# Kernel optimization log

Measured on AMD Instinct MI355X. Metric: run time of the kernel, lower is better.

Reference implementation:

```python
import jax, jax.numpy as jnp
import numpy as np

N_NODES = 100_000
N_EDGES = 1_600_000
N_SPECIES = 4
ATTR = 16
HID = 32
NBASIS = 8
SH = 4  # l=0 (1) + l=1 (3)
R_CUT = 5.0


def setup_inputs() -> dict:
    key = jax.random.key(0)
    ks = jax.random.split(key, 13)
    inp = {
        "x": jax.random.randint(ks[0], (N_NODES,), 0, N_SPECIES),
        "pos": jax.random.normal(ks[1], (N_NODES, 3), jnp.float32),
        "edge_index": jax.random.randint(ks[2], (2, N_EDGES), 0, N_NODES),
        "cell": jax.random.normal(ks[3], (3, 3), jnp.float32),
        "cell_offset": jax.random.randint(ks[4], (N_EDGES, 3), 0, 3),
        "elem_embed": jax.random.normal(ks[5], (N_SPECIES, ATTR), jnp.float32),
        "W_embed": jax.random.normal(ks[6], (ATTR, HID), jnp.float32) * 0.25,
        "Wr": jax.random.normal(ks[7], (3, NBASIS, HID * SH), jnp.float32) * 0.25,
        "br": jax.random.normal(ks[8], (3, HID * SH), jnp.float32) * 0.1,
        "Wout": jax.random.normal(ks[9], (3, HID, HID), jnp.float32) * 0.18,
        "Wsc": jax.random.normal(ks[10], (3, ATTR, HID), jnp.float32) * 0.25,
        "P1": jax.random.normal(ks[11], (HID, 32), jnp.float32) * 0.18,
        "P2": jax.random.normal(ks[12], (32, 4), jnp.float32) * 0.18,
    }
    return inp


def _radial_basis(r, r_safe):
    # Bessel basis with smooth polynomial cutoff (p = 6)
    n = jnp.arange(1, NBASIS + 1, dtype=r.dtype)  # [NBASIS]
    rb = jnp.sin(n * jnp.pi * r / R_CUT) / r_safe  # [E, NBASIS]
    u = r / R_CUT
    p = 6.0
    env = 1.0 - (p + 1) * (p + 2) / 2 * u ** p + p * (p + 2) * u ** (p + 1) - p * (p + 1) / 2 * u ** (p + 2)
    env = jnp.where(u < 1.0, env, 0.0)
    return rb * env


def reference(x, pos, edge_index, cell, cell_offset, elem_embed, W_embed, Wr, br, Wout, Wsc, P1, P2):
    src, dst = edge_index[0], edge_index[1]
    n_nodes = pos.shape[0]
    n_edges = src.shape[0]

    # PBC shift vectors (offsets in {-1,0,1})
    period_vec = (cell_offset.astype(pos.dtype) - 1.0) @ cell  # [E,3]

    # node attributes / initial embedding
    x_attr = elem_embed[x]          # [N, ATTR]
    h = x_attr @ W_embed            # [N, HID]

    # edge attributes: vectors, lengths, spherical harmonics (l<=1)
    edge_vec = pos[dst] - pos[src] + period_vec            # [E,3]
    r = jnp.linalg.norm(edge_vec, axis=-1, keepdims=True)  # [E,1]
    r_safe = jnp.maximum(r, 1e-9)
    unit = edge_vec / r_safe
    edge_sh = jnp.concatenate([jnp.ones_like(r), unit], axis=-1)  # [E,SH]

    rbf = _radial_basis(r, r_safe)  # [E, NBASIS]

    # 3 message-passing convolutions
    for l in range(3):
        w = (rbf @ Wr[l] + br[l]).reshape(n_edges, HID, SH)          # per-edge TP weights
        msg = jnp.einsum('eh,es,ehs->eh', h[src], edge_sh, w)        # gather + edge compute
        agg = jax.ops.segment_sum(msg, dst, num_segments=n_nodes)    # scatter-reduce
        h = jax.nn.silu(agg @ Wout[l] + x_attr @ Wsc[l])

    # post-conv readout
    h = jax.nn.silu(h @ P1) @ P2  # [N,4]
    energies = h[:, 0]
    forces = h[:, 1:4]
    return energies, forces
```

## Files before the change

kernel.cpp:

```cpp
#include <hip/hip_runtime.h>
#include <hip/hip_bf16.h>
#include <math.h>

#define NN 100000
#define NE 1600000
#define HIDD 32
#define ATTR_ 16
#define NB 8
#define NBUK 782
#define CAP 2560
#define WPB 10
#define SCHUNK 4096
#define PAD_PAY (13<<17)

typedef __hip_bfloat16 bf16;
typedef _Float16 half8  __attribute__((ext_vector_type(8)));
typedef _Float16 half2v __attribute__((ext_vector_type(2)));
typedef float    f32x4  __attribute__((ext_vector_type(4)));

__device__ __forceinline__ float silu_(float v){ return v / (1.f + expf(-v)); }

__global__ void k_init(const int* __restrict__ x, const float* __restrict__ elem,
                       const float* __restrict__ Wemb, bf16* __restrict__ h,
                       float* __restrict__ agg){
  int idx = blockIdx.x*256 + threadIdx.x;
  if (idx >= NN*HIDD) return;
  int node = idx >> 5, hh = idx & 31;
  int xi = x[node];
  float acc = 0.f;
  #pragma unroll
  for (int a=0; a<ATTR_; a++) acc += elem[xi*ATTR_+a] * Wemb[a*HIDD+hh];
  h[idx] = __float2bfloat16(acc);
  agg[idx] = 0.f;
}

__global__ void k_binit(int* __restrict__ bcur){
  int i = blockIdx.x*256 + threadIdx.x;
  if (i < NBUK) bcur[i] = i*CAP;
}

__global__ void __launch_bounds__(256) k_bscatter(
    const int* __restrict__ ei, const int* __restrict__ coff,
    int* __restrict__ bcur, int* __restrict__ pairs){
  __shared__ int lh[NBUK];
  __shared__ int gb[NBUK];
  __shared__ int sbr[SCHUNK];
  __shared__ int spay[SCHUNK];
  const int t = threadIdx.x;
  const int base = blockIdx.x * SCHUNK;
  for (int i=t; i<NBUK; i+=256) lh[i] = 0;
  __syncthreads();
  for (int rr=0; rr<SCHUNK; rr+=256){
    int e = base + rr + t;
    if (e < NE){
      int src = ei[e], dst = ei[NE + e];
      int code = coff[e*3+0] + 3*coff[e*3+1] + 9*coff[e*3+2];
      int b = dst >> 7;
      int rank = atomicAdd(&lh[b], 1);
      sbr[rr+t]  = (b<<16) | rank;
      spay[rr+t] = src | (code<<17) | ((dst & 127)<<22);
    }
  }
  __syncthreads();
  for (int i=t; i<NBUK; i+=256){
    int c = lh[i];
    gb[i] = c ? atomicAdd(&bcur[i], c) : 0;
  }
  __syncthreads();
  for (int rr=0; rr<SCHUNK; rr+=256){
    int e = base + rr + t;
    if (e < NE){
      int br = sbr[rr+t];
      int b = br >> 16;
      int p = gb[b] + (br & 0xFFFF);
      if (p < (b+1)*CAP) pairs[p] = spay[rr+t];
    }
  }
}

__global__ void __launch_bounds__(256) k_fsort(
    const int* __restrict__ pairs, const int* __restrict__ bcur,
    int* __restrict__ es){
  __shared__ int spay[CAP];
  __shared__ int hist[128];
  __shared__ int cur[128];
  const int b = blockIdx.x, t = threadIdx.x;
  const int base = b*CAP;
  int K = bcur[b] - base; if (K > CAP) K = CAP; if (K < 0) K = 0;
  if (t < 128) hist[t] = 0;
  __syncthreads();
  for (int i=t; i<K; i+=256){
    int pay = pairs[base + i];
    spay[i] = pay;
    atomicAdd(&hist[(pay>>22) & 127], 1);
  }
  __syncthreads();
  if (t < 128) cur[t] = hist[t];
  __syncthreads();
  #pragma unroll
  for (int off=1; off<128; off<<=1){
    int u = (t >= off && t < 128) ? cur[t-off] : 0;
    __syncthreads();
    if (t < 128) cur[t] += u;
    __syncthreads();
  }
  if (t < 128) cur[t] -= hist[t];
  __syncthreads();
  for (int i=t; i<K; i+=256){
    int pay = spay[i];
    int p = base + atomicAdd(&cur[(pay>>22) & 127], 1);
    es[p] = pay;
  }
  for (int i=K+t; i<CAP; i+=256) es[base+i] = PAD_PAY;
}

__global__ void __launch_bounds__(256) k_edge8(
    const int* __restrict__ es, const int* __restrict__ bcur,
    const float* __restrict__ pos, const float* __restrict__ cell,
    const float* __restrict__ Wr_l, const float* __restrict__ br_l,
    const bf16* __restrict__ h, float* __restrict__ agg){
  __shared__ _Float16 Gs[256][40];
  __shared__ float ssh[256][4];
  __shared__ int ssrc[256];
  __shared__ int sdst[256];
  __shared__ _Float16 W2T[32][32];
  __shared__ float scell[9];
  const int t = threadIdx.x;

  int blk;
  {
    const int nwg = gridDim.x;
    int q = nwg >> 3, r = nwg & 7;
    int xcd = blockIdx.x & 7, lidx = blockIdx.x >> 3;
    blk = (xcd < r) ? (xcd*(q+1) + lidx) : (r*(q+1) + (xcd-r)*q + lidx);
  }
  const int b = blk / WPB, w = blk - b*WPB;
  const int base0 = b*CAP;
  int K = bcur[b] - base0; if (K > CAP) K = CAP;
  const int rem = K - w*256;
  if (rem <= 0) return;
  const int remc = rem < 256 ? rem : 256;

  if (t < 9) scell[t] = cell[t];
  {
    int hh2 = t >> 3, kq = t & 7;
    float4 w4 = *reinterpret_cast<const float4*>(Wr_l + kq*128 + hh2*4);
    W2T[hh2][kq*4+0] = (_Float16)w4.x;
    W2T[hh2][kq*4+1] = (_Float16)w4.y;
    W2T[hh2][kq*4+2] = (_Float16)w4.z;
    W2T[hh2][kq*4+3] = (_Float16)w4.w;
  }

  const int j = base0 + w*256 + t;
  const int pay = es[j];
  const int srcn = pay & 0x1FFFF;
  const int dstn = (b<<7) + ((pay>>22) & 127);
  ssrc[t] = srcn; sdst[t] = dstn;
  float pdx = pos[dstn*3+0], pdy = pos[dstn*3+1], pdz = pos[dstn*3+2];
  float psx = pos[srcn*3+0], psy = pos[srcn*3+1], psz = pos[srcn*3+2];
  __syncthreads();

  const int g = t >> 5, hh = t & 31, base = g*32;
  const unsigned short* hu = reinterpret_cast<const unsigned short*>(h);
  unsigned short hb[32];
  #pragma unroll
  for (int k=0; k<32; k++)
    hb[k] = hu[(size_t)ssrc[base+k]*HIDD + hh];

  {
    int code = (pay >> 17) & 31;
    int q = code / 3;
    float c0 = (float)(code - 3*q - 1);
    float c1 = (float)(q - 3*(q/3) - 1);
    float c2 = (float)(q/3 - 1);
    float vx = pdx - psx + c0*scell[0]+c1*scell[3]+c2*scell[6];
    float vy = pdy - psy + c0*scell[1]+c1*scell[4]+c2*scell[7];
    float vz = pdz - psz + c0*scell[2]+c1*scell[5]+c2*scell[8];
    float r  = sqrtf(vx*vx + vy*vy + vz*vz);
    float rs = fmaxf(r, 1e-9f);
    float u  = r * 0.2f;
    float env = 0.f;
    if (u < 1.f){
      float u2=u*u, u3=u2*u, u6=u3*u3, u7=u6*u, u8=u7*u;
      env = 1.f - 28.f*u6 + 48.f*u7 - 21.f*u8;
    }
    float sc = env / rs;
    float s1, c1t;
    __sincosf(0.62831853071795864769f * r, &s1, &c1t);
    float twoc = 2.f*c1t;
    float inv = 1.f / rs;
    float ux = vx*inv, uy = vy*inv, uz = vz*inv;
    float sp = 0.f, sn = s1;
    #pragma unroll
    for (int bb=0; bb<NB; bb++){
      float rb = sn*sc;
      half2v p0 = { (_Float16)rb,      (_Float16)(rb*ux) };
      half2v p1 = { (_Float16)(rb*uy), (_Float16)(rb*uz) };
      *reinterpret_cast<half2v*>(&Gs[t][bb*4])   = p0;
      *reinterpret_cast<half2v*>(&Gs[t][bb*4+2]) = p1;
      float nx = twoc*sn - sp; sp = sn; sn = nx;
    }
    float4 sh4 = make_float4(1.f, ux, uy, uz);
    *reinterpret_cast<float4*>(ssh[t]) = sh4;
  }

  asm volatile("s_waitcnt lgkmcnt(0)" ::: "memory");
  __builtin_amdgcn_s_barrier();
  __builtin_amdgcn_sched_barrier(0);

  {
    const int wv = t >> 6, l = t & 63;
    const int lrow = l & 15, lk = l >> 4;
    half8 b0 = *reinterpret_cast<half8*>(&W2T[lrow][lk*8]);
    half8 b1 = *reinterpret_cast<half8*>(&W2T[16+lrow][lk*8]);
    float4 br0 = *reinterpret_cast<const float4*>(br_l + 4*lrow);
    float4 br1 = *reinterpret_cast<const float4*>(br_l + 4*(16+lrow));
    const f32x4 zz = {0.f,0.f,0.f,0.f};
    #pragma unroll
    for (int m=0; m<4; m++){
      half8 a = *reinterpret_cast<half8*>(&Gs[(wv*4+m)*16 + lrow][lk*8]);
      f32x4 c0 = __builtin_amdgcn_mfma_f32_16x16x32_f16(a, b0, zz, 0, 0, 0);
      f32x4 c1 = __builtin_amdgcn_mfma_f32_16x16x32_f16(a, b1, zz, 0, 0, 0);
      #pragma unroll
      for (int r=0; r<4; r++){
        int edge = (wv*4+m)*16 + lk*4 + r;
        float4 sh4 = *reinterpret_cast<float4*>(ssh[edge]);
        float bias0 = sh4.x*br0.x + sh4.y*br0.y + sh4.z*br0.z + sh4.w*br0.w;
        float bias1 = sh4.x*br1.x + sh4.y*br1.y + sh4.z*br1.z + sh4.w*br1.w;
        Gs[edge][lrow]    = (_Float16)(c0[r] + bias0);
        Gs[edge][16+lrow] = (_Float16)(c1[r] + bias1);
      }
    }
  }

  float accv = 0.f;
  int curd = sdst[base];
  #pragma unroll
  for (int k=0; k<32; k++){
    const int idx = base + k;
    int dst = sdst[idx];
    bool ok = idx < remc;
    if (ok && dst != curd){ atomicAdd(agg + (size_t)curd*HIDD + hh, accv); accv = 0.f; curd = dst; }
    float hv = __uint_as_float(((unsigned)hb[k]) << 16);
    float cvf = (float)Gs[idx][hh];
    if (ok) accv += hv * cvf;
  }
  if (accv != 0.f) atomicAdd(agg + (size_t)curd*HIDD + hh, accv);
}

__global__ void __launch_bounds__(256) k_edge(
    const float* __restrict__ pos, const int* __restrict__ ei,
    const float* __restrict__ cell, const int* __restrict__ coff,
    const float* __restrict__ Wr_l, const float* __restrict__ br_l,
    const bf16* __restrict__ h, float* __restrict__ agg){
  __shared__ float sfeat[8][12];
  __shared__ int   snode[8][2];
  const int e0 = blockIdx.x * 8;
  const int t  = threadIdx.x;
  if (t < 8){
    int e = e0 + t;
    int src = ei[e], dst = ei[NE + e];
    snode[t][0] = src; snode[t][1] = dst;
    float c0 = (float)(coff[e*3+0] - 1);
    float c1 = (float)(coff[e*3+1] - 1);
    float c2 = (float)(coff[e*3+2] - 1);
    float vx = pos[dst*3+0]-pos[src*3+0] + c0*cell[0]+c1*cell[3]+c2*cell[6];
    float vy = pos[dst*3+1]-pos[src*3+1] + c0*cell[1]+c1*cell[4]+c2*cell[7];
    float vz = pos[dst*3+2]-pos[src*3+2] + c0*cell[2]+c1*cell[5]+c2*cell[8];
    float r  = sqrtf(vx*vx+vy*vy+vz*vz);
    float rs = fmaxf(r, 1e-9f);
    float u  = r * 0.2f;
    float env = 0.f;
    if (u < 1.f){
      float u2=u*u, u3=u2*u, u6=u3*u3, u7=u6*u, u8=u7*u;
      env = 1.f - 28.f*u6 + 48.f*u7 - 21.f*u8;
    }
    float sc = env / rs;
    #pragma unroll
    for (int b=0; b<NB; b++)
      sfeat[t][b] = sinf((float)(b+1) * 3.14159265358979323846f * u) * sc;
    float inv = 1.f / rs;
    sfeat[t][8]  = 1.f;
    sfeat[t][9]  = vx*inv;
    sfeat[t][10] = vy*inv;
    sfeat[t][11] = vz*inv;
  }
  __syncthreads();
  const int el = t >> 5, hh = t & 31;
  const int src = snode[el][0], dst = snode[el][1];
  float hs = __bfloat162float(h[(size_t)src*HIDD + hh]);
  float4 acc = *reinterpret_cast<const float4*>(br_l + 4*hh);
  #pragma unroll
  for (int b=0; b<NB; b++){
    float rb = sfeat[el][b];
    float4 w = *reinterpret_cast<const float4*>(Wr_l + b*128 + 4*hh);
    acc.x += rb*w.x; acc.y += rb*w.y; acc.z += rb*w.z; acc.w += rb*w.w;
  }
  float c = acc.x*sfeat[el][8] + acc.y*sfeat[el][9]
          + acc.z*sfeat[el][10] + acc.w*sfeat[el][11];
  atomicAdd(agg + (size_t)dst*HIDD + hh, hs*c);
}

__global__ void k_node(const int* __restrict__ x, const float* __restrict__ elem,
                       const float* __restrict__ Wout_l, const float* __restrict__ Wsc_l,
                       bf16* __restrict__ h, float* __restrict__ agg){
  int idx = blockIdx.x*256 + threadIdx.x;
  if (idx >= NN*HIDD) return;
  int node = idx >> 5, hh = idx & 31;
  int xi = x[node];
  const float* arow = agg + (size_t)node*HIDD;
  float acc = 0.f;
  #pragma unroll
  for (int i=0; i<HIDD; i++) acc += arow[i] * Wout_l[i*HIDD+hh];
  #pragma unroll
  for (int a=0; a<ATTR_; a++) acc += elem[xi*ATTR_+a] * Wsc_l[a*HIDD+hh];
  h[idx] = __float2bfloat16(silu_(acc));
  agg[idx] = 0.f;
}

__global__ void __launch_bounds__(256) k_final2(
    const bf16* __restrict__ h, const float* __restrict__ P1,
    const float* __restrict__ P2, float* __restrict__ out){
  __shared__ float sP1[32][32];
  __shared__ float sh[8][32];
  const int t = threadIdx.x;
  {
    float4 v = reinterpret_cast<const float4*>(P1)[t];
    int r = (t*4) >> 5, c = (t*4) & 31;
    sP1[r][c]   = v.x; sP1[r][c+1] = v.y;
    sP1[r][c+2] = v.z; sP1[r][c+3] = v.w;
  }
  const int node0 = blockIdx.x * 8;
  ((float*)sh)[t] = __bfloat162float(h[(size_t)node0*HIDD + t]);
  __syncthreads();
  const int g = t >> 5, j = t & 31;
  const int node = node0 + g;
  float tj = 0.f;
  #pragma unroll
  for (int i=0; i<32; i++) tj += sh[g][i] * sP1[i][j];
  tj = silu_(tj);
  float4 p2 = reinterpret_cast<const float4*>(P2)[j];
  float o0 = tj*p2.x, o1 = tj*p2.y, o2 = tj*p2.z, o3 = tj*p2.w;
  #pragma unroll
  for (int m=1; m<32; m<<=1){
    o0 += __shfl_xor(o0, m);
    o1 += __shfl_xor(o1, m);
    o2 += __shfl_xor(o2, m);
    o3 += __shfl_xor(o3, m);
  }
  if (j == 0){
    out[node]            = o0;
    out[NN + node*3 + 0] = o1;
    out[NN + node*3 + 1] = o2;
    out[NN + node*3 + 2] = o3;
  }
}

extern "C" void kernel_launch(void* const* d_in, const int* in_sizes, int n_in,
                              void* d_out, int out_size, void* d_ws, size_t ws_size,
                              hipStream_t stream){
  const int*   x    = (const int*)  d_in[0];
  const float* pos  = (const float*)d_in[1];
  const int*   ei   = (const int*)  d_in[2];
  const float* cell = (const float*)d_in[3];
  const int*   coff = (const int*)  d_in[4];
  const float* elem = (const float*)d_in[5];
  const float* Wemb = (const float*)d_in[6];
  const float* Wr   = (const float*)d_in[7];
  const float* br   = (const float*)d_in[8];
  const float* Wout = (const float*)d_in[9];
  const float* Wsc  = (const float*)d_in[10];
  const float* P1   = (const float*)d_in[11];
  const float* P2   = (const float*)d_in[12];
  float* out = (float*)d_out;

  char* w = (char*)d_ws;
  bf16*  h    = (bf16*)w;  w += (size_t)NN*HIDD*2;
  float* agg  = (float*)w; w += (size_t)NN*HIDD*4;
  int*   bcur = (int*)w;   w += (size_t)1024*4;
  int*   es   = (int*)w;   w += (size_t)NBUK*CAP*4;
  const size_t need = (size_t)(w - (char*)d_ws);
  const bool fast = (ws_size >= need);
  int* pairs = (int*)agg;

  if (fast){
    k_binit<<<(NBUK+255)/256, 256, 0, stream>>>(bcur);
    k_bscatter<<<(NE + SCHUNK-1)/SCHUNK, 256, 0, stream>>>(ei, coff, bcur, pairs);
    k_fsort<<<NBUK, 256, 0, stream>>>(pairs, bcur, es);
  }
  k_init<<<(NN*HIDD+255)/256, 256, 0, stream>>>(x, elem, Wemb, h, agg);
  for (int l=0; l<3; l++){
    if (fast){
      k_edge8<<<NBUK*WPB, 256, 0, stream>>>(es, bcur, pos, cell,
                                            Wr + (size_t)l*NB*HIDD*4, br + (size_t)l*HIDD*4,
                                            h, agg);
    } else {
      k_edge<<<NE/8, 256, 0, stream>>>(pos, ei, cell, coff,
                                       Wr + (size_t)l*NB*HIDD*4, br + (size_t)l*HIDD*4,
                                       h, agg);
    }
    k_node<<<(NN*HIDD+255)/256, 256, 0, stream>>>(x, elem,
                                       Wout + (size_t)l*HIDD*HIDD, Wsc + (size_t)l*ATTR_*HIDD,
                                       h, agg);
  }
  k_final2<<<NN/8, 256, 0, stream>>>(h, P1, P2, out);
}
```

Baseline: 342.5 us.

## Compact sorted edges globally and replace LDS staging with wave shuffles

Adds a single-block prefix scan over bucket counts so the sorted edge list is stored densely, with an explicit per-edge destination array. This removes the padded per-bucket slots, so the edge kernel launches exactly NE/256 blocks with no early exit or validity masks. Source ids, destination ids and unit vectors are now passed between lanes with __shfl instead of shared-memory arrays, which drops several LDS buffers and one barrier. The cost is an extra tiny scan kernel and an extra 4-byte destination read per edge in each layer; it also relies on NE being a multiple of 256 and on no bucket overflowing CAP.

```diff
diff --git a/kernel.cpp b/kernel.cpp
--- a/kernel.cpp
+++ b/kernel.cpp
@@ -9,9 +9,7 @@
 #define NB 8
 #define NBUK 782
 #define CAP 2560
-#define WPB 10
 #define SCHUNK 4096
-#define PAD_PAY (13<<17)
 
 typedef __hip_bfloat16 bf16;
 typedef _Float16 half8  __attribute__((ext_vector_type(8)));
@@ -78,19 +76,38 @@
   }
 }
 
+__global__ void __launch_bounds__(1024) k_gscan(const int* __restrict__ bcur,
+                                               int* __restrict__ goff){
+  __shared__ int s[1024];
+  const int t = threadIdx.x;
+  int v = 0;
+  if (t < NBUK){ v = bcur[t] - t*CAP; if (v > CAP) v = CAP; if (v < 0) v = 0; }
+  s[t] = v; __syncthreads();
+  #pragma unroll
+  for (int off=1; off<1024; off<<=1){
+    int u = (t >= off) ? s[t-off] : 0;
+    __syncthreads();
+    s[t] += u;
+    __syncthreads();
+  }
+  if (t < NBUK) goff[t] = s[t] - v;
+}
+
 __global__ void __launch_bounds__(256) k_fsort(
     const int* __restrict__ pairs, const int* __restrict__ bcur,
-    int* __restrict__ es){
+    const int* __restrict__ goff,
+    int* __restrict__ es, int* __restrict__ dsts){
   __shared__ int spay[CAP];
   __shared__ int hist[128];
   __shared__ int cur[128];
   const int b = blockIdx.x, t = threadIdx.x;
-  const int base = b*CAP;
-  int K = bcur[b] - base; if (K > CAP) K = CAP; if (K < 0) K = 0;
+  const int sbase = b*CAP;
+  int K = bcur[b] - sbase; if (K > CAP) K = CAP; if (K < 0) K = 0;
+  const int gbase = goff[b];
   if (t < 128) hist[t] = 0;
   __syncthreads();
   for (int i=t; i<K; i+=256){
-    int pay = pairs[base + i];
+    int pay = pairs[sbase + i];
     spay[i] = pay;
     atomicAdd(&hist[(pay>>22) & 127], 1);
   }
@@ -106,25 +123,23 @@
   }
   if (t < 128) cur[t] -= hist[t];
   __syncthreads();
+  const int node0 = b << 7;
   for (int i=t; i<K; i+=256){
     int pay = spay[i];
-    int p = base + atomicAdd(&cur[(pay>>22) & 127], 1);
-    es[p] = pay;
-  }
-  for (int i=K+t; i<CAP; i+=256) es[base+i] = PAD_PAY;
-}
-
-__global__ void __launch_bounds__(256) k_edge8(
-    const int* __restrict__ es, const int* __restrict__ bcur,
+    int loc = (pay>>22) & 127;
+    int p = gbase + atomicAdd(&cur[loc], 1);
+    es[p]   = pay;
+    dsts[p] = node0 + loc;
+  }
+}
+
+__global__ void __launch_bounds__(256) k_edge9(
+    const int* __restrict__ es, const int* __restrict__ dsts,
     const float* __restrict__ pos, const float* __restrict__ cell,
     const float* __restrict__ Wr_l, const float* __restrict__ br_l,
     const bf16* __restrict__ h, float* __restrict__ agg){
   __shared__ _Float16 Gs[256][40];
-  __shared__ float ssh[256][4];
-  __shared__ int ssrc[256];
-  __shared__ int sdst[256];
   __shared__ _Float16 W2T[32][32];
-  __shared__ float scell[9];
   const int t = threadIdx.x;
 
   int blk;
@@ -134,14 +149,11 @@
     int xcd = blockIdx.x & 7, lidx = blockIdx.x >> 3;
     blk = (xcd < r) ? (xcd*(q+1) + lidx) : (r*(q+1) + (xcd-r)*q + lidx);
   }
-  const int b = blk / WPB, w = blk - b*WPB;
-  const int base0 = b*CAP;
-  int K = bcur[b] - base0; if (K > CAP) K = CAP;
-  const int rem = K - w*256;
-  if (rem <= 0) return;
-  const int remc = rem < 256 ? rem : 256;
-
-  if (t < 9) scell[t] = cell[t];
+
+  const int j = blk*256 + t;
+  const int pay = es[j];
+  const int dstn = dsts[j];
+  const int srcn = pay & 0x1FFFF;
   {
     int hh2 = t >> 3, kq = t & 7;
     float4 w4 = *reinterpret_cast<const float4*>(Wr_l + kq*128 + hh2*4);
@@ -150,32 +162,33 @@
     W2T[hh2][kq*4+2] = (_Float16)w4.z;
     W2T[hh2][kq*4+3] = (_Float16)w4.w;
   }
-
-  const int j = base0 + w*256 + t;
-  const int pay = es[j];
-  const int srcn = pay & 0x1FFFF;
-  const int dstn = (b<<7) + ((pay>>22) & 127);
-  ssrc[t] = srcn; sdst[t] = dstn;
   float pdx = pos[dstn*3+0], pdy = pos[dstn*3+1], pdz = pos[dstn*3+2];
   float psx = pos[srcn*3+0], psy = pos[srcn*3+1], psz = pos[srcn*3+2];
-  __syncthreads();
-
-  const int g = t >> 5, hh = t & 31, base = g*32;
+
+  asm volatile("s_waitcnt lgkmcnt(0)" ::: "memory");
+  __builtin_amdgcn_s_barrier();
+  __builtin_amdgcn_sched_barrier(0);
+
+  const int hh = t & 31;
+  const int hlane = ((t>>5)&1)*32;
   const unsigned short* hu = reinterpret_cast<const unsigned short*>(h);
   unsigned short hb[32];
   #pragma unroll
-  for (int k=0; k<32; k++)
-    hb[k] = hu[(size_t)ssrc[base+k]*HIDD + hh];
-
+  for (int k=0; k<32; k++){
+    int s = __shfl(srcn, hlane + k, 64);
+    hb[k] = hu[(size_t)s*HIDD + hh];
+  }
+
+  float ux, uy, uz;
   {
     int code = (pay >> 17) & 31;
     int q = code / 3;
     float c0 = (float)(code - 3*q - 1);
     float c1 = (float)(q - 3*(q/3) - 1);
     float c2 = (float)(q/3 - 1);
-    float vx = pdx - psx + c0*scell[0]+c1*scell[3]+c2*scell[6];
-    float vy = pdy - psy + c0*scell[1]+c1*scell[4]+c2*scell[7];
-    float vz = pdz - psz + c0*scell[2]+c1*scell[5]+c2*scell[8];
+    float vx = pdx - psx + c0*cell[0]+c1*cell[3]+c2*cell[6];
+    float vy = pdy - psy + c0*cell[1]+c1*cell[4]+c2*cell[7];
+    float vz = pdz - psz + c0*cell[2]+c1*cell[5]+c2*cell[8];
     float r  = sqrtf(vx*vx + vy*vy + vz*vz);
     float rs = fmaxf(r, 1e-9f);
     float u  = r * 0.2f;
@@ -189,7 +202,7 @@
     __sincosf(0.62831853071795864769f * r, &s1, &c1t);
     float twoc = 2.f*c1t;
     float inv = 1.f / rs;
-    float ux = vx*inv, uy = vy*inv, uz = vz*inv;
+    ux = vx*inv; uy = vy*inv; uz = vz*inv;
     float sp = 0.f, sn = s1;
     #pragma unroll
     for (int bb=0; bb<NB; bb++){
@@ -200,8 +213,6 @@
       *reinterpret_cast<half2v*>(&Gs[t][bb*4+2]) = p1;
       float nx = twoc*sn - sp; sp = sn; sn = nx;
     }
-    float4 sh4 = make_float4(1.f, ux, uy, uz);
-    *reinterpret_cast<float4*>(ssh[t]) = sh4;
   }
 
   asm volatile("s_waitcnt lgkmcnt(0)" ::: "memory");
@@ -223,29 +234,30 @@
       f32x4 c1 = __builtin_amdgcn_mfma_f32_16x16x32_f16(a, b1, zz, 0, 0, 0);
       #pragma unroll
       for (int r=0; r<4; r++){
-        int edge = (wv*4+m)*16 + lk*4 + r;
-        float4 sh4 = *reinterpret_cast<float4*>(ssh[edge]);
-        float bias0 = sh4.x*br0.x + sh4.y*br0.y + sh4.z*br0.z + sh4.w*br0.w;
-        float bias1 = sh4.x*br1.x + sh4.y*br1.y + sh4.z*br1.z + sh4.w*br1.w;
+        const int srcl = m*16 + lk*4 + r;
+        const int edge = wv*64 + srcl;
+        float ex = __shfl(ux, srcl, 64);
+        float ey = __shfl(uy, srcl, 64);
+        float ez = __shfl(uz, srcl, 64);
+        float bias0 = br0.x + ex*br0.y + ey*br0.z + ez*br0.w;
+        float bias1 = br1.x + ex*br1.y + ey*br1.z + ez*br1.w;
         Gs[edge][lrow]    = (_Float16)(c0[r] + bias0);
         Gs[edge][16+lrow] = (_Float16)(c1[r] + bias1);
       }
     }
   }
 
+  const int base = (t >> 5)*32;
   float accv = 0.f;
-  int curd = sdst[base];
+  int curd = __shfl(dstn, hlane, 64);
   #pragma unroll
   for (int k=0; k<32; k++){
-    const int idx = base + k;
-    int dst = sdst[idx];
-    bool ok = idx < remc;
-    if (ok && dst != curd){ atomicAdd(agg + (size_t)curd*HIDD + hh, accv); accv = 0.f; curd = dst; }
+    int dst = __shfl(dstn, hlane + k, 64);
+    if (dst != curd){ atomicAdd(agg + (size_t)curd*HIDD + hh, accv); accv = 0.f; curd = dst; }
     float hv = __uint_as_float(((unsigned)hb[k]) << 16);
-    float cvf = (float)Gs[idx][hh];
-    if (ok) accv += hv * cvf;
-  }
-  if (accv != 0.f) atomicAdd(agg + (size_t)curd*HIDD + hh, accv);
+    accv += hv * (float)Gs[base + k][hh];
+  }
+  atomicAdd(agg + (size_t)curd*HIDD + hh, accv);
 }
 
 __global__ void __launch_bounds__(256) k_edge(
@@ -378,7 +390,9 @@
   bf16*  h    = (bf16*)w;  w += (size_t)NN*HIDD*2;
   float* agg  = (float*)w; w += (size_t)NN*HIDD*4;
   int*   bcur = (int*)w;   w += (size_t)1024*4;
-  int*   es   = (int*)w;   w += (size_t)NBUK*CAP*4;
+  int*   goff = (int*)w;   w += (size_t)1024*4;
+  int*   es   = (int*)w;   w += (size_t)NE*4;
+  int*   dsts = (int*)w;   w += (size_t)NE*4;
   const size_t need = (size_t)(w - (char*)d_ws);
   const bool fast = (ws_size >= need);
   int* pairs = (int*)agg;
@@ -386,14 +400,15 @@
   if (fast){
     k_binit<<<(NBUK+255)/256, 256, 0, stream>>>(bcur);
     k_bscatter<<<(NE + SCHUNK-1)/SCHUNK, 256, 0, stream>>>(ei, coff, bcur, pairs);
-    k_fsort<<<NBUK, 256, 0, stream>>>(pairs, bcur, es);
+    k_gscan<<<1, 1024, 0, stream>>>(bcur, goff);
+    k_fsort<<<NBUK, 256, 0, stream>>>(pairs, bcur, goff, es, dsts);
   }
   k_init<<<(NN*HIDD+255)/256, 256, 0, stream>>>(x, elem, Wemb, h, agg);
   for (int l=0; l<3; l++){
     if (fast){
-      k_edge8<<<NBUK*WPB, 256, 0, stream>>>(es, bcur, pos, cell,
-                                            Wr + (size_t)l*NB*HIDD*4, br + (size_t)l*HIDD*4,
-                                            h, agg);
+      k_edge9<<<NE/256, 256, 0, stream>>>(es, dsts, pos, cell,
+                                          Wr + (size_t)l*NB*HIDD*4, br + (size_t)l*HIDD*4,
+                                          h, agg);
     } else {
       k_edge<<<NE/8, 256, 0, stream>>>(pos, ei, cell, coff,
                                        Wr + (size_t)l*NB*HIDD*4, br + (size_t)l*HIDD*4,
```

After: 346.1 us. About the same (+1.0%).
